# Kernel tuning notes

Hardware: AMD Instinct MI355X
Metric: run time of the kernel (lower is better)

The kernel has to match this reference:

```python
import jax, jax.numpy as jnp
import numpy as np

HEADS = 8
DIM = 512
DIM_HEAD = DIM // 8        # 64
M = DIM // 2               # 256 landmarks
PINV_ITERS = 6
KERNEL = 33                # residual depthwise conv kernel (33,1)


def moore_penrose_pinv(x, iters):
    # x: [b, h, m, m]; Newton-Schulz style iterative pseudoinverse (lucidrains impl)
    abs_x = jnp.abs(x)
    col = abs_x.sum(axis=-1)
    row = abs_x.sum(axis=-2)
    z = jnp.swapaxes(x, -1, -2) / (jnp.max(col) * jnp.max(row))
    I = jnp.eye(x.shape[-1], dtype=x.dtype)
    for _ in range(iters):
        xz = x @ z
        z = 0.25 * z @ (13.0 * I - xz @ (15.0 * I - xz @ (7.0 * I - xz)))
    return z


def setup_inputs() -> dict:
    key = jax.random.key(0)
    ks = jax.random.split(key, 5)
    b, n, dim = 4, 8192, DIM
    x = jax.random.normal(ks[0], (b, n, dim), dtype=jnp.float32)
    # to_qkv: Linear(dim, 3*inner_dim, bias=False); inner_dim = heads*dim_head = dim
    w_qkv = jax.random.normal(ks[1], (dim, 3 * dim), dtype=jnp.float32) / np.sqrt(dim)
    # to_out: Linear(inner_dim, dim) with bias (dropout = identity in eval)
    w_out = jax.random.normal(ks[2], (dim, dim), dtype=jnp.float32) / np.sqrt(dim)
    b_out = jax.random.normal(ks[3], (dim,), dtype=jnp.float32) * 0.01
    # res_conv: Conv2d(heads, heads, (33,1), padding=(16,0), groups=heads, bias=False)
    conv_w = jax.random.normal(ks[4], (HEADS, 1, KERNEL, 1), dtype=jnp.float32) / np.sqrt(KERNEL)
    return {"x": x, "w_qkv": w_qkv, "w_out": w_out, "b_out": b_out, "conv_w": conv_w}


def nystrom_attention(x, w_qkv, w_out, b_out, conv_w):
    b, n, dim = x.shape
    h, d, m = HEADS, DIM_HEAD, M
    # pad front so seq len divisible by num_landmarks (no-op for n=8192, m=256)
    pad = (m - n % m) % m
    xp = jnp.pad(x, ((0, 0), (pad, 0), (0, 0)))
    np_ = n + pad

    qkv = xp @ w_qkv                                   # [b, np, 3*dim]
    q, k, v = jnp.split(qkv, 3, axis=-1)
    to_heads = lambda t: t.reshape(b, np_, h, d).transpose(0, 2, 1, 3)  # [b,h,np,d]
    q, k, v = to_heads(q), to_heads(k), to_heads(v)
    q = q * (d ** -0.5)

    l = np_ // m                                       # tokens per landmark
    pool = lambda t: t.reshape(b, h, m, l, d).mean(axis=3)  # [b,h,m,d]
    q_l, k_l = pool(q), pool(k)

    attn1 = jax.nn.softmax(jnp.einsum('bhnd,bhmd->bhnm', q, k_l), axis=-1)    # [b,h,np,m]
    attn2 = jax.nn.softmax(jnp.einsum('bhid,bhjd->bhij', q_l, k_l), axis=-1)  # [b,h,m,m]
    attn3 = jax.nn.softmax(jnp.einsum('bhmd,bhnd->bhmn', q_l, k), axis=-1)    # [b,h,m,np]

    attn2_inv = moore_penrose_pinv(attn2, PINV_ITERS)
    out = (attn1 @ attn2_inv) @ (attn3 @ v)            # [b,h,np,d]

    # depthwise conv residual over the sequence axis, per head
    res = jax.lax.conv_general_dilated(
        v, conv_w, window_strides=(1, 1),
        padding=((KERNEL // 2, KERNEL // 2), (0, 0)),
        dimension_numbers=('NCHW', 'OIHW', 'NCHW'),
        feature_group_count=h)
    out = out + res

    out = out.transpose(0, 2, 1, 3).reshape(b, np_, dim)
    out = out @ w_out + b_out
    return out[:, -n:]


def reference(x, w_qkv, w_out, b_out, conv_w):
    return x + nystrom_attention(x, w_qkv, w_out, b_out, conv_w)
```

## Files before the change

kernel.cpp:

```cpp
#include <hip/hip_runtime.h>


#define N_SEQ 8192
#define DMODEL 512
#define NHEAD 8
#define DHEAD 64
#define NLAND 256
#define BH 32

typedef unsigned short u16;
typedef __attribute__((ext_vector_type(8))) short bh8;
typedef __attribute__((ext_vector_type(4))) float fx4;

__device__ __forceinline__ float bf2f(u16 u) { return __uint_as_float(((unsigned)u) << 16); }
__device__ __forceinline__ u16 f2bf(float f) {
    unsigned x = __float_as_uint(f);
    return (u16)((x + 0x7fffu + ((x >> 16) & 1u)) >> 16);
}
__device__ __forceinline__ fx4 mfma16(bh8 a, bh8 b, fx4 c) {
    return __builtin_amdgcn_mfma_f32_16x16x32_bf16(a, b, c, 0, 0, 0);
}

__global__ void detect_kernel(const u16* __restrict__ X, unsigned* flag_out)
{
    __shared__ int cnt;
    if (threadIdx.x == 0) cnt = 0;
    __syncthreads();
    u16 u = X[threadIdx.x * 2];
    int e = (u >> 7) & 0xFF;
    int insane = (u != 0) && (e < 90 || e > 140);
    atomicAdd(&cnt, insane);
    __syncthreads();
    if (threadIdx.x == 0) flag_out[0] = (cnt > 64) ? 1u : 0u;
}

__global__ __launch_bounds__(256) void convert_kernel(
    const void* __restrict__ in, u16* __restrict__ out, int n, const unsigned* __restrict__ flag)
{
    int i = blockIdx.x * 256 + threadIdx.x;
    if (i >= n) return;
    if (flag[0]) out[i] = f2bf(((const float*)in)[i]);
    else         out[i] = ((const u16*)in)[i];
}

__global__ __launch_bounds__(256) void wtrans_kernel(
    const void* __restrict__ in, u16* __restrict__ out, int rows, int cols,
    const unsigned* __restrict__ flag)
{
    int idx = blockIdx.x * 256 + threadIdx.x;
    if (idx >= rows * cols) return;
    int r = idx / cols, c = idx % cols;
    float v = flag[0] ? ((const float*)in)[idx] : bf2f(((const u16*)in)[idx]);
    out[(size_t)c * rows + r] = f2bf(v);
}

__global__ __launch_bounds__(256) void f2b_kernel(const float* __restrict__ in, u16* __restrict__ out, int n)
{
    int i = blockIdx.x * 256 + threadIdx.x;
    if (i < n) out[i] = f2bf(in[i]);
}

__global__ __launch_bounds__(256) void qkv_mfma_kernel(
    const u16* __restrict__ X, const u16* __restrict__ WT,
    u16* __restrict__ Q, u16* __restrict__ K, u16* __restrict__ VT)
{
    __shared__ u16 Xs[128 * 40];
    __shared__ u16 Ws[128 * 40];
    const int tid = threadIdx.x;
    const int wave = tid >> 6, lane = tid & 63;
    const int wrow = (wave >> 1) * 64, wcol = (wave & 1) * 64;
    const int i0 = blockIdx.x * 128;
    const int j0 = blockIdx.y * 128;
    const int lr = tid >> 2, lk = (tid & 3) * 8;
    const int lm = lane & 15, lq = lane >> 4;
    fx4 acc[4][4];
#pragma unroll
    for (int a = 0; a < 4; ++a)
#pragma unroll
        for (int b = 0; b < 4; ++b) acc[a][b] = (fx4){0.f, 0.f, 0.f, 0.f};

    for (int k0 = 0; k0 < DMODEL; k0 += 32) {
        uint4 x0 = *(const uint4*)(X + (size_t)(i0 + lr) * DMODEL + k0 + lk);
        uint4 x1 = *(const uint4*)(X + (size_t)(i0 + 64 + lr) * DMODEL + k0 + lk);
        uint4 w0 = *(const uint4*)(WT + (size_t)(j0 + lr) * DMODEL + k0 + lk);
        uint4 w1 = *(const uint4*)(WT + (size_t)(j0 + 64 + lr) * DMODEL + k0 + lk);
        __syncthreads();
        *(uint4*)(Xs + lr * 40 + lk) = x0;
        *(uint4*)(Xs + (64 + lr) * 40 + lk) = x1;
        *(uint4*)(Ws + lr * 40 + lk) = w0;
        *(uint4*)(Ws + (64 + lr) * 40 + lk) = w1;
        __syncthreads();
        bh8 xf[4], wf[4];
#pragma unroll
        for (int im = 0; im < 4; ++im)
            xf[im] = *(const bh8*)(Xs + (wrow + im * 16 + lm) * 40 + lq * 8);
#pragma unroll
        for (int in = 0; in < 4; ++in)
            wf[in] = *(const bh8*)(Ws + (wcol + in * 16 + lm) * 40 + lq * 8);
#pragma unroll
        for (int im = 0; im < 4; ++im)
#pragma unroll
            for (int in = 0; in < 4; ++in)
                acc[im][in] = mfma16(wf[in], xf[im], acc[im][in]);
    }
#pragma unroll
    for (int im = 0; im < 4; ++im) {
        int m = i0 + wrow + im * 16 + lm;
        int bb = m >> 13, ns = m & (N_SEQ - 1);
#pragma unroll
        for (int in = 0; in < 4; ++in) {
            int nn = j0 + wcol + in * 16 + (lq << 2);
            int which = nn >> 9;
            int h = (nn >> 6) & 7;
            int d = nn & 63;
            if (which == 2) {
                size_t vb = (size_t)(bb * NHEAD + h) * DHEAD;
#pragma unroll
                for (int cc = 0; cc < 4; ++cc)
                    VT[(vb + d + cc) * N_SEQ + ns] = f2bf(acc[im][in][cc]);
            } else {
                u16* dst = (which == 0) ? Q : K;
                float sc = (which == 0) ? 0.125f : 1.f;
                ushort4 o;
                o.x = f2bf(acc[im][in][0] * sc); o.y = f2bf(acc[im][in][1] * sc);
                o.z = f2bf(acc[im][in][2] * sc); o.w = f2bf(acc[im][in][3] * sc);
                *(ushort4*)(dst + ((size_t)(bb * NHEAD + h) * N_SEQ + ns) * DHEAD + d) = o;
            }
        }
    }
}

__global__ __launch_bounds__(64) void pool_kernel(
    const u16* __restrict__ Q, const u16* __restrict__ K,
    float* __restrict__ QL, float* __restrict__ KL,
    u16* __restrict__ QLb, u16* __restrict__ KLb)
{
    int m = blockIdx.x, bh = blockIdx.y, d = threadIdx.x;
    size_t base = ((size_t)bh * N_SEQ + m * 32) * DHEAD + d;
    float sq = 0.f, sk = 0.f;
#pragma unroll
    for (int i = 0; i < 32; ++i) {
        sq += bf2f(Q[base + i * DHEAD]);
        sk += bf2f(K[base + i * DHEAD]);
    }
    size_t ob = ((size_t)bh * NLAND + m) * DHEAD + d;
    sq *= (1.f / 32.f); sk *= (1.f / 32.f);
    QL[ob] = sq; KL[ob] = sk;
    QLb[ob] = f2bf(sq); KLb[ob] = f2bf(sk);
}

__global__ __launch_bounds__(256) void attn2_kernel(
    const float* __restrict__ QL, const float* __restrict__ KL, float* __restrict__ A2)
{
    __shared__ float qrow[64];
    __shared__ float red[256];
    int i = blockIdx.x, bh = blockIdx.y, j = threadIdx.x;
    if (j < 64) qrow[j] = QL[((size_t)bh * NLAND + i) * DHEAD + j];
    __syncthreads();
    const float* kr = KL + ((size_t)bh * NLAND + j) * DHEAD;
    float lg = 0.f;
#pragma unroll
    for (int d = 0; d < 64; ++d) lg += qrow[d] * kr[d];
    red[j] = lg; __syncthreads();
    for (int s = 128; s > 0; s >>= 1) { if (j < s) red[j] = fmaxf(red[j], red[j + s]); __syncthreads(); }
    float mx = red[0]; __syncthreads();
    float p = __expf(lg - mx);
    red[j] = p; __syncthreads();
    for (int s = 128; s > 0; s >>= 1) { if (j < s) red[j] += red[j + s]; __syncthreads(); }
    float sum = red[0];
    A2[((size_t)bh * NLAND + i) * NLAND + j] = p / sum;
}

__global__ void init_scal_kernel(unsigned* scal) { if (threadIdx.x < 2) scal[threadIdx.x] = 0u; }

__global__ __launch_bounds__(256) void absmax_kernel(const float* __restrict__ A2, unsigned* scal)
{
    __shared__ float red[256];
    int bh = blockIdx.x, t = threadIdx.x;
    const float* Ab = A2 + (size_t)bh * 65536;
    float cs = 0.f, rs = 0.f;
    for (int j = 0; j < 256; ++j) cs += fabsf(Ab[t * 256 + j]);
    for (int i = 0; i < 256; ++i) rs += fabsf(Ab[i * 256 + t]);
    red[t] = cs; __syncthreads();
    for (int s = 128; s > 0; s >>= 1) { if (t < s) red[t] = fmaxf(red[t], red[t + s]); __syncthreads(); }
    if (t == 0) atomicMax(scal + 0, __float_as_uint(red[0]));
    __syncthreads();
    red[t] = rs; __syncthreads();
    for (int s = 128; s > 0; s >>= 1) { if (t < s) red[t] = fmaxf(red[t], red[t + s]); __syncthreads(); }
    if (t == 0) atomicMax(scal + 1, __float_as_uint(red[0]));
}

__global__ __launch_bounds__(256) void z0_kernel(
    const float* __restrict__ A2, const unsigned* __restrict__ scal,
    u16* __restrict__ zb, u16* __restrict__ zbT)
{
    float inv = 1.f / (__uint_as_float(scal[0]) * __uint_as_float(scal[1]));
    size_t idx = (size_t)blockIdx.x * 256 + threadIdx.x;
    size_t bh = idx >> 16;
    int r = (int)(idx & 65535);
    int i = r >> 8, j = r & 255;
    zb[idx]  = f2bf(A2[(bh << 16) + (size_t)j * 256 + i] * inv);
    zbT[idx] = f2bf(A2[idx] * inv);
}

__global__ __launch_bounds__(256) void bgemm_mfma_kernel(
    const u16* __restrict__ A, const u16* __restrict__ BT,
    u16* __restrict__ Cn, u16* __restrict__ Ct, const u16* __restrict__ E,
    int N, long sB, long sCn, long sCt, float sc, float alpha, float beta, int wn, int wt)
{
    __shared__ u16 As[64 * 40];
    __shared__ u16 Bs[64 * 40];
    const int tid = threadIdx.x;
    const int wave = tid >> 6, lane = tid & 63;
    const int wm = (wave >> 1) * 32, wnn = (wave & 1) * 32;
    const int i0 = blockIdx.x * 64, j0 = blockIdx.y * 64, bh = blockIdx.z;
    const u16* Ab = A + (size_t)bh * 65536;
    const u16* Bb = BT + (size_t)bh * sB;
    const int lr = tid >> 2, lk = (tid & 3) * 8;
    const int lm = lane & 15, lq = lane >> 4;
    fx4 acc[2][2];
#pragma unroll
    for (int a = 0; a < 2; ++a)
#pragma unroll
        for (int b = 0; b < 2; ++b) acc[a][b] = (fx4){0.f, 0.f, 0.f, 0.f};

    for (int k0 = 0; k0 < 256; k0 += 32) {
        uint4 a4 = *(const uint4*)(Ab + (size_t)(i0 + lr) * 256 + k0 + lk);
        uint4 b4 = *(const uint4*)(Bb + (size_t)(j0 + lr) * 256 + k0 + lk);
        __syncthreads();
        *(uint4*)(As + lr * 40 + lk) = a4;
        *(uint4*)(Bs + lr * 40 + lk) = b4;
        __syncthreads();
        bh8 lf[2], rf[2];
#pragma unroll
        for (int im = 0; im < 2; ++im)
            lf[im] = *(const bh8*)(As + (wm + im * 16 + lm) * 40 + lq * 8);
#pragma unroll
        for (int in = 0; in < 2; ++in)
            rf[in] = *(const bh8*)(Bs + (wnn + in * 16 + lm) * 40 + lq * 8);
#pragma unroll
        for (int im = 0; im < 2; ++im)
#pragma unroll
            for (int in = 0; in < 2; ++in)
                acc[im][in] = mfma16(lf[im], rf[in], acc[im][in]);
    }
#pragma unroll
    for (int im = 0; im < 2; ++im) {
#pragma unroll
        for (int in = 0; in < 2; ++in) {
            int n = j0 + wnn + in * 16 + lm;
            int m0 = i0 + wm + im * 16 + (lq << 2);
            float c[4];
#pragma unroll
            for (int r = 0; r < 4; ++r) {
                int m = m0 + r;
                float x = beta * acc[im][in][r];
                if (alpha != 0.f)
                    x += alpha * bf2f(E[(size_t)bh * 65536 + (size_t)m * 256 + n]);
                if (m == n) x += sc;
                c[r] = x;
            }
            if (wn) {
#pragma unroll
                for (int r = 0; r < 4; ++r)
                    Cn[(size_t)bh * sCn + (size_t)(m0 + r) * N + n] = f2bf(c[r]);
            }
            if (wt) {
                ushort4 o;
                o.x = f2bf(c[0]); o.y = f2bf(c[1]); o.z = f2bf(c[2]); o.w = f2bf(c[3]);
                *(ushort4*)(Ct + (size_t)bh * sCt + (size_t)n * 256 + m0) = o;
            }
        }
    }
}

__global__ __launch_bounds__(256) void attn3v_mfma_kernel(
    const u16* __restrict__ QLb, const u16* __restrict__ Kb,
    const u16* __restrict__ VTb, u16* __restrict__ PO, float* __restrict__ ML)
{
    __shared__ u16 Pl[4][32 * 72];
    const int tid = threadIdx.x;
    const int wave = tid >> 6, lane = tid & 63;
    const int q = lane >> 4, l15 = lane & 15;
    const int m0 = blockIdx.x * 32;
    const int part = blockIdx.y * 4 + wave;
    const int bh = blockIdx.z;
    const int nbase = part * 512;
    u16* Pw = Pl[wave];
    bh8 qf[2][2];
#pragma unroll
    for (int mt = 0; mt < 2; ++mt)
#pragma unroll
        for (int ks = 0; ks < 2; ++ks)
            qf[mt][ks] = *(const bh8*)(QLb + ((size_t)bh * NLAND + m0 + mt * 16 + l15) * DHEAD + ks * 32 + q * 8);
    float M[2] = {-1e30f, -1e30f};
    float L[2] = {0.f, 0.f};
    fx4 O[2][4];
#pragma unroll
    for (int mt = 0; mt < 2; ++mt)
#pragma unroll
        for (int dt = 0; dt < 4; ++dt) O[mt][dt] = (fx4){0.f, 0.f, 0.f, 0.f};

    for (int c = 0; c < 8; ++c) {
        const int n0 = nbase + c * 64;
        fx4 S[4][2];
#pragma unroll
        for (int nt = 0; nt < 4; ++nt)
#pragma unroll
            for (int mt = 0; mt < 2; ++mt) S[nt][mt] = (fx4){0.f, 0.f, 0.f, 0.f};
#pragma unroll
        for (int ks = 0; ks < 2; ++ks)
#pragma unroll
            for (int nt = 0; nt < 4; ++nt) {
                bh8 kf = *(const bh8*)(Kb + ((size_t)bh * N_SEQ + n0 + nt * 16 + l15) * DHEAD + ks * 32 + q * 8);
                S[nt][0] = mfma16(kf, qf[0][ks], S[nt][0]);
                S[nt][1] = mfma16(kf, qf[1][ks], S[nt][1]);
            }
#pragma unroll
        for (int mt = 0; mt < 2; ++mt) {
            float cm = -1e30f;
#pragma unroll
            for (int nt = 0; nt < 4; ++nt)
#pragma unroll
                for (int r = 0; r < 4; ++r) cm = fmaxf(cm, S[nt][mt][r]);
            cm = fmaxf(cm, __shfl_xor(cm, 16));
            cm = fmaxf(cm, __shfl_xor(cm, 32));
            float Mn = fmaxf(M[mt], cm);
            float al = __expf(M[mt] - Mn);
            M[mt] = Mn;
            L[mt] *= al;
#pragma unroll
            for (int dt = 0; dt < 4; ++dt) {
                O[mt][dt][0] *= al; O[mt][dt][1] *= al;
                O[mt][dt][2] *= al; O[mt][dt][3] *= al;
            }
            float ps = 0.f;
#pragma unroll
            for (int nt = 0; nt < 4; ++nt)
#pragma unroll
                for (int r = 0; r < 4; ++r) {
                    float p = __expf(S[nt][mt][r] - Mn);
                    ps += p;
                    Pw[(mt * 16 + l15) * 72 + nt * 16 + q * 4 + r] = f2bf(p);
                }
            ps += __shfl_xor(ps, 16);
            ps += __shfl_xor(ps, 32);
            L[mt] += ps;
        }
#pragma unroll
        for (int ks = 0; ks < 2; ++ks) {
            bh8 pf[2];
#pragma unroll
            for (int mt = 0; mt < 2; ++mt)
                pf[mt] = *(const bh8*)(Pw + (mt * 16 + l15) * 72 + ks * 32 + q * 8);
#pragma unroll
            for (int dt = 0; dt < 4; ++dt) {
                bh8 vf = *(const bh8*)(VTb + ((size_t)bh * DHEAD + dt * 16 + l15) * N_SEQ + n0 + ks * 32 + q * 8);
                O[0][dt] = mfma16(vf, pf[0], O[0][dt]);
                O[1][dt] = mfma16(vf, pf[1], O[1][dt]);
            }
        }
    }
#pragma unroll
    for (int mt = 0; mt < 2; ++mt) {
        size_t mrow = (size_t)(bh * 16 + part) * NLAND + m0 + mt * 16 + l15;
#pragma unroll
        for (int dt = 0; dt < 4; ++dt) {
            ushort4 o;
            o.x = f2bf(O[mt][dt][0]); o.y = f2bf(O[mt][dt][1]);
            o.z = f2bf(O[mt][dt][2]); o.w = f2bf(O[mt][dt][3]);
            *(ushort4*)(PO + mrow * DHEAD + dt * 16 + q * 4) = o;
        }
        if (q == 0) { ML[mrow * 2] = M[mt]; ML[mrow * 2 + 1] = L[mt]; }
    }
}

__global__ __launch_bounds__(64) void combine_kernel(
    const u16* __restrict__ PO, const float* __restrict__ ML, u16* __restrict__ W3VT)
{
    int m = blockIdx.x, bh = blockIdx.y, d = threadIdx.x;
    float Mg = -1e30f;
#pragma unroll
    for (int p = 0; p < 16; ++p)
        Mg = fmaxf(Mg, ML[((size_t)(bh * 16 + p) * NLAND + m) * 2]);
    float denom = 0.f, o = 0.f;
#pragma unroll
    for (int p = 0; p < 16; ++p) {
        size_t ix = (size_t)(bh * 16 + p) * NLAND + m;
        float w = __expf(ML[ix * 2] - Mg);
        denom += ML[ix * 2 + 1] * w;
        o += bf2f(PO[ix * DHEAD + d]) * w;
    }
    W3VT[((size_t)bh * DHEAD + d) * NLAND + m] = f2bf(o / denom);
}

__global__ __launch_bounds__(256) void outheads_mfma_kernel(
    const u16* __restrict__ Qb, const u16* __restrict__ KLb,
    const u16* __restrict__ WMT, const u16* __restrict__ VTb,
    const u16* __restrict__ CW, u16* __restrict__ Y)
{
    __shared__ u16 Pl[32 * 264];
    __shared__ u16 vsh[64 * 72];
    __shared__ float wmax[4][32], wsum[4][32];
    __shared__ float cws[33];
    const int tid = threadIdx.x;
    const int wave = tid >> 6, lane = tid & 63;
    const int q = lane >> 4, l15 = lane & 15;
    const int bh = blockIdx.y;
    const int bb = bh >> 3, h = bh & 7;
    const int n0 = blockIdx.x * 32;
#pragma unroll
    for (int e = 0; e < 16; ++e) {
        int d = wave * 16 + e;
        int gn = n0 - 16 + lane;
        u16 v = (gn >= 0 && gn < N_SEQ) ? VTb[((size_t)bh * DHEAD + d) * N_SEQ + gn] : (u16)0;
        vsh[lane * 72 + d] = v;
    }
    if (tid < 33) cws[tid] = bf2f(CW[h * 33 + tid]);
    fx4 S[2][4];
#pragma unroll
    for (int nt = 0; nt < 2; ++nt)
#pragma unroll
        for (int mt = 0; mt < 4; ++mt) S[nt][mt] = (fx4){0.f, 0.f, 0.f, 0.f};
#pragma unroll
    for (int ks = 0; ks < 2; ++ks) {
        bh8 qfr[2];
#pragma unroll
        for (int nt = 0; nt < 2; ++nt)
            qfr[nt] = *(const bh8*)(Qb + ((size_t)bh * N_SEQ + n0 + nt * 16 + l15) * DHEAD + ks * 32 + q * 8);
#pragma unroll
        for (int mt = 0; mt < 4; ++mt) {
            bh8 kf = *(const bh8*)(KLb + ((size_t)bh * NLAND + wave * 64 + mt * 16 + l15) * DHEAD + ks * 32 + q * 8);
            S[0][mt] = mfma16(qfr[0], kf, S[0][mt]);
            S[1][mt] = mfma16(qfr[1], kf, S[1][mt]);
        }
    }
#pragma unroll
    for (int nt = 0; nt < 2; ++nt)
#pragma unroll
        for (int r = 0; r < 4; ++r) {
            float pm = -1e30f;
#pragma unroll
            for (int mt = 0; mt < 4; ++mt) pm = fmaxf(pm, S[nt][mt][r]);
            pm = fmaxf(pm, __shfl_xor(pm, 1));
            pm = fmaxf(pm, __shfl_xor(pm, 2));
            pm = fmaxf(pm, __shfl_xor(pm, 4));
            pm = fmaxf(pm, __shfl_xor(pm, 8));
            if (l15 == 0) wmax[wave][nt * 16 + q * 4 + r] = pm;
        }
    __syncthreads();
#pragma unroll
    for (int nt = 0; nt < 2; ++nt)
#pragma unroll
        for (int r = 0; r < 4; ++r) {
            int nl = nt * 16 + q * 4 + r;
            float Mfull = fmaxf(fmaxf(wmax[0][nl], wmax[1][nl]), fmaxf(wmax[2][nl], wmax[3][nl]));
            float ps = 0.f;
#pragma unroll
            for (int mt = 0; mt < 4; ++mt) {
                float p = __expf(S[nt][mt][r] - Mfull);
                ps += p;
                Pl[nl * 264 + wave * 64 + mt * 16 + l15] = f2bf(p);
            }
            ps += __shfl_xor(ps, 1);
            ps += __shfl_xor(ps, 2);
            ps += __shfl_xor(ps, 4);
            ps += __shfl_xor(ps, 8);
            if (l15 == 0) wsum[wave][nl] = ps;
        }
    __syncthreads();
    fx4 O[2];
    O[0] = (fx4){0.f, 0.f, 0.f, 0.f};
    O[1] = (fx4){0.f, 0.f, 0.f, 0.f};
#pragma unroll
    for (int ks = 0; ks < 8; ++ks) {
        bh8 af = *(const bh8*)(WMT + ((size_t)bh * DHEAD + wave * 16 + l15) * NLAND + ks * 32 + q * 8);
#pragma unroll
        for (int nt = 0; nt < 2; ++nt) {
            bh8 pf = *(const bh8*)(Pl + (nt * 16 + l15) * 264 + ks * 32 + q * 8);
            O[nt] = mfma16(af, pf, O[nt]);
        }
    }
#pragma unroll
    for (int nt = 0; nt < 2; ++nt) {
        int nl = nt * 16 + l15;
        float inv = 1.f / (wsum[0][nl] + wsum[1][nl] + wsum[2][nl] + wsum[3][nl]);
        fx4 v = O[nt];
        v[0] *= inv; v[1] *= inv; v[2] *= inv; v[3] *= inv;
#pragma unroll
        for (int t = 0; t < 33; ++t) {
            float w = cws[t];
            const u16* vp = vsh + (nl + t) * 72 + wave * 16 + q * 4;
            v[0] += w * bf2f(vp[0]); v[1] += w * bf2f(vp[1]);
            v[2] += w * bf2f(vp[2]); v[3] += w * bf2f(vp[3]);
        }
        ushort4 o;
        o.x = f2bf(v[0]); o.y = f2bf(v[1]); o.z = f2bf(v[2]); o.w = f2bf(v[3]);
        *(ushort4*)(Y + ((size_t)bb * N_SEQ + n0 + nl) * DMODEL + h * DHEAD + wave * 16 + q * 4) = o;
    }
}

__global__ __launch_bounds__(256) void final_mfma_kernel(
    const u16* __restrict__ Y, const u16* __restrict__ WT,
    const u16* __restrict__ Bias, const u16* __restrict__ X, void* __restrict__ Out,
    const unsigned* __restrict__ flag)
{
    __shared__ u16 Xs[128 * 40];
    __shared__ u16 Ws[128 * 40];
    const int tid = threadIdx.x;
    const int wave = tid >> 6, lane = tid & 63;
    const int wrow = (wave >> 1) * 64, wcol = (wave & 1) * 64;
    const int i0 = blockIdx.x * 128;
    const int j0 = blockIdx.y * 128;
    const int lr = tid >> 2, lk = (tid & 3) * 8;
    const int lm = lane & 15, lq = lane >> 4;
    const unsigned isf32 = flag[0];
    fx4 acc[4][4];
#pragma unroll
    for (int a = 0; a < 4; ++a)
#pragma unroll
        for (int b = 0; b < 4; ++b) acc[a][b] = (fx4){0.f, 0.f, 0.f, 0.f};

    for (int k0 = 0; k0 < DMODEL; k0 += 32) {
        uint4 x0 = *(const uint4*)(Y + (size_t)(i0 + lr) * DMODEL + k0 + lk);
        uint4 x1 = *(const uint4*)(Y + (size_t)(i0 + 64 + lr) * DMODEL + k0 + lk);
        uint4 w0 = *(const uint4*)(WT + (size_t)(j0 + lr) * DMODEL + k0 + lk);
        uint4 w1 = *(const uint4*)(WT + (size_t)(j0 + 64 + lr) * DMODEL + k0 + lk);
        __syncthreads();
        *(uint4*)(Xs + lr * 40 + lk) = x0;
        *(uint4*)(Xs + (64 + lr) * 40 + lk) = x1;
        *(uint4*)(Ws + lr * 40 + lk) = w0;
        *(uint4*)(Ws + (64 + lr) * 40 + lk) = w1;
        __syncthreads();
        bh8 xf[4], wf[4];
#pragma unroll
        for (int im = 0; im < 4; ++im)
            xf[im] = *(const bh8*)(Xs + (wrow + im * 16 + lm) * 40 + lq * 8);
#pragma unroll
        for (int in = 0; in < 4; ++in)
            wf[in] = *(const bh8*)(Ws + (wcol + in * 16 + lm) * 40 + lq * 8);
#pragma unroll
        for (int im = 0; im < 4; ++im)
#pragma unroll
            for (int in = 0; in < 4; ++in)
                acc[im][in] = mfma16(wf[in], xf[im], acc[im][in]);
    }
#pragma unroll
    for (int im = 0; im < 4; ++im) {
        int m = i0 + wrow + im * 16 + lm;
#pragma unroll
        for (int in = 0; in < 4; ++in) {
            int nn = j0 + wcol + in * 16 + (lq << 2);
            ushort4 b4 = *(const ushort4*)(Bias + nn);
            ushort4 x4 = *(const ushort4*)(X + (size_t)m * DMODEL + nn);
            float c0 = acc[im][in][0] + bf2f(b4.x) + bf2f(x4.x);
            float c1 = acc[im][in][1] + bf2f(b4.y) + bf2f(x4.y);
            float c2 = acc[im][in][2] + bf2f(b4.z) + bf2f(x4.z);
            float c3 = acc[im][in][3] + bf2f(b4.w) + bf2f(x4.w);
            if (isf32) {
                *(float4*)((float*)Out + (size_t)m * DMODEL + nn) = make_float4(c0, c1, c2, c3);
            } else {
                ushort4 o;
                o.x = f2bf(c0); o.y = f2bf(c1); o.z = f2bf(c2); o.w = f2bf(c3);
                *(ushort4*)((u16*)Out + (size_t)m * DMODEL + nn) = o;
            }
        }
    }
}

extern "C" void kernel_launch(void* const* d_in, const int* in_sizes, int n_in,
                              void* d_out, int out_size, void* d_ws, size_t ws_size,
                              hipStream_t stream)
{
    (void)in_sizes; (void)n_in; (void)out_size; (void)ws_size;
    char* ws = (char*)d_ws;
    u16*   Xc    = (u16*)(ws + 0);
    u16*   WqkvT = (u16*)(ws + 33554432);
    u16*   WoutT = (u16*)(ws + 35127296);
    u16*   Boutc = (u16*)(ws + 35651584);
    u16*   CWc   = (u16*)(ws + 35652608);
    u16*   Qb    = (u16*)(ws + 35653632);
    u16*   Kb    = (u16*)(ws + 69208064);
    u16*   VTb   = (u16*)(ws + 102762496);
    float* QL    = (float*)(ws + 136316928);
    float* KL    = (float*)(ws + 138414080);
    u16*   QLb   = (u16*)(ws + 140511232);
    u16*   KLb   = (u16*)(ws + 141559808);
    u16*   W3VT  = (u16*)(ws + 142608384);
    u16*   WMT   = (u16*)(ws + 143656960);
    u16*   A2b   = (u16*)(ws + 144705536);
    u16*   zA    = (u16*)(ws + 148899840);
    u16*   zAT   = (u16*)(ws + 153094144);
    float* A2    = (float*)(ws + 157288448);
    u16*   PO    = (u16*)(ws + 157288448);
    float* ML    = (float*)(ws + 174065664);
    u16*   zB    = (u16*)(ws + 165677056);
    u16*   zBT   = (u16*)(ws + 169871360);
    u16*   xz    = (u16*)(ws + 174065664);
    u16*   xzT   = (u16*)(ws + 178259968);
    u16*   t2T   = (u16*)(ws + 182454272);
    u16*   t3T   = (u16*)(ws + 186648576);
    u16*   Yb    = (u16*)(ws + 157288448);
    unsigned* SCAL = (unsigned*)(ws + 190842880);

    detect_kernel<<<1, 256, 0, stream>>>((const u16*)d_in[0], SCAL + 2);
    convert_kernel<<<65536, 256, 0, stream>>>(d_in[0], Xc, 16777216, SCAL + 2);
    wtrans_kernel<<<3072, 256, 0, stream>>>(d_in[1], WqkvT, 512, 1536, SCAL + 2);
    wtrans_kernel<<<1024, 256, 0, stream>>>(d_in[2], WoutT, 512, 512, SCAL + 2);
    convert_kernel<<<2, 256, 0, stream>>>(d_in[3], Boutc, 512, SCAL + 2);
    convert_kernel<<<2, 256, 0, stream>>>(d_in[4], CWc, 264, SCAL + 2);

    qkv_mfma_kernel<<<dim3(256, 12), 256, 0, stream>>>(Xc, WqkvT, Qb, Kb, VTb);
    pool_kernel<<<dim3(256, BH), 64, 0, stream>>>(Qb, Kb, QL, KL, QLb, KLb);
    attn2_kernel<<<dim3(256, BH), 256, 0, stream>>>(QL, KL, A2);
    init_scal_kernel<<<1, 64, 0, stream>>>(SCAL);
    absmax_kernel<<<32, 256, 0, stream>>>(A2, SCAL);
    z0_kernel<<<8192, 256, 0, stream>>>(A2, SCAL, zA, zAT);
    f2b_kernel<<<8192, 256, 0, stream>>>(A2, A2b, 2097152);

    attn3v_mfma_kernel<<<dim3(8, 4, BH), 256, 0, stream>>>(QLb, Kb, VTb, PO, ML);
    combine_kernel<<<dim3(256, BH), 64, 0, stream>>>(PO, ML, W3VT);

    u16 *z = zA, *zT = zAT, *zn = zB, *znT = zBT;
    for (int it = 0; it < 6; ++it) {
        bgemm_mfma_kernel<<<dim3(4, 4, 32), 256, 0, stream>>>(
            A2b, zT, xz, xzT, A2b, 256, 65536, 65536, 65536, 0.f, 0.f, 1.f, 1, 1);
        bgemm_mfma_kernel<<<dim3(4, 4, 32), 256, 0, stream>>>(
            xz, xzT, xz, t2T, xz, 256, 65536, 65536, 65536, 15.f, -7.f, 1.f, 0, 1);
        bgemm_mfma_kernel<<<dim3(4, 4, 32), 256, 0, stream>>>(
            xz, t2T, xz, t3T, xz, 256, 65536, 65536, 65536, 13.f, 0.f, -1.f, 0, 1);
        bgemm_mfma_kernel<<<dim3(4, 4, 32), 256, 0, stream>>>(
            z, t3T, zn, znT, xz, 256, 65536, 65536, 65536, 0.f, 0.f, 0.25f, 1, 1);
        u16* t;
        t = z; z = zn; zn = t;
        t = zT; zT = znT; znT = t;
    }
    bgemm_mfma_kernel<<<dim3(4, 1, 32), 256, 0, stream>>>(
        z, W3VT, WMT, WMT, xz, 64, 16384, 16384, 16384, 0.f, 0.f, 1.f, 0, 1);
    outheads_mfma_kernel<<<dim3(256, BH), 256, 0, stream>>>(Qb, KLb, WMT, VTb, CWc, Yb);
    final_mfma_kernel<<<dim3(256, 4), 256, 0, stream>>>(Yb, WoutT, Boutc, Xc, d_out, SCAL + 2);
}
```

Before: 847.5 us.

## Use direct global-to-LDS loads with swizzle in GEMMs and split out residual conv

The QKV and output GEMMs now use global_load_lds with an XOR-swizzled 64-wide K tile instead of register-staged loads into padded shared memory. The depthwise residual conv moves into a separate conv_kernel that writes RT into the now-unused K buffer. The output-heads kernel handles 64 tokens per block and just adds the precomputed RT. This cuts register staging and recomputation of the conv, at the cost of an extra kernel launch and an extra round-trip of the conv result through global memory.

```diff
diff --git a/kernel.cpp b/kernel.cpp
--- a/kernel.cpp
+++ b/kernel.cpp
@@ -19,6 +19,11 @@
 }
 __device__ __forceinline__ fx4 mfma16(bh8 a, bh8 b, fx4 c) {
     return __builtin_amdgcn_mfma_f32_16x16x32_bf16(a, b, c, 0, 0, 0);
+}
+__device__ __forceinline__ void gload16(u16* lds, const u16* g) {
+    __builtin_amdgcn_global_load_lds(
+        (const __attribute__((address_space(1))) unsigned int*)g,
+        (__attribute__((address_space(3))) unsigned int*)lds, 16, 0, 0);
 }
 
 __global__ void detect_kernel(const u16* __restrict__ X, unsigned* flag_out)
@@ -64,44 +69,48 @@
     const u16* __restrict__ X, const u16* __restrict__ WT,
     u16* __restrict__ Q, u16* __restrict__ K, u16* __restrict__ VT)
 {
-    __shared__ u16 Xs[128 * 40];
-    __shared__ u16 Ws[128 * 40];
+    __shared__ u16 Xs[128 * 64];
+    __shared__ u16 Ws[128 * 64];
     const int tid = threadIdx.x;
     const int wave = tid >> 6, lane = tid & 63;
     const int wrow = (wave >> 1) * 64, wcol = (wave & 1) * 64;
     const int i0 = blockIdx.x * 128;
     const int j0 = blockIdx.y * 128;
-    const int lr = tid >> 2, lk = (tid & 3) * 8;
+    const int la = lane >> 3, lb = lane & 7;
     const int lm = lane & 15, lq = lane >> 4;
+    const int sw = lm & 7;
+    const int sc = (lb ^ la) * 8;
     fx4 acc[4][4];
 #pragma unroll
     for (int a = 0; a < 4; ++a)
 #pragma unroll
         for (int b = 0; b < 4; ++b) acc[a][b] = (fx4){0.f, 0.f, 0.f, 0.f};
 
-    for (int k0 = 0; k0 < DMODEL; k0 += 32) {
-        uint4 x0 = *(const uint4*)(X + (size_t)(i0 + lr) * DMODEL + k0 + lk);
-        uint4 x1 = *(const uint4*)(X + (size_t)(i0 + 64 + lr) * DMODEL + k0 + lk);
-        uint4 w0 = *(const uint4*)(WT + (size_t)(j0 + lr) * DMODEL + k0 + lk);
-        uint4 w1 = *(const uint4*)(WT + (size_t)(j0 + 64 + lr) * DMODEL + k0 + lk);
+    for (int k0 = 0; k0 < DMODEL; k0 += 64) {
         __syncthreads();
-        *(uint4*)(Xs + lr * 40 + lk) = x0;
-        *(uint4*)(Xs + (64 + lr) * 40 + lk) = x1;
-        *(uint4*)(Ws + lr * 40 + lk) = w0;
-        *(uint4*)(Ws + (64 + lr) * 40 + lk) = w1;
+#pragma unroll
+        for (int jj = 0; jj < 4; ++jj) {
+            int rb = wave * 32 + jj * 8;
+            gload16(Xs + rb * 64, X + (size_t)(i0 + rb + la) * DMODEL + k0 + sc);
+            gload16(Ws + rb * 64, WT + (size_t)(j0 + rb + la) * DMODEL + k0 + sc);
+        }
         __syncthreads();
-        bh8 xf[4], wf[4];
-#pragma unroll
-        for (int im = 0; im < 4; ++im)
-            xf[im] = *(const bh8*)(Xs + (wrow + im * 16 + lm) * 40 + lq * 8);
-#pragma unroll
-        for (int in = 0; in < 4; ++in)
-            wf[in] = *(const bh8*)(Ws + (wcol + in * 16 + lm) * 40 + lq * 8);
-#pragma unroll
-        for (int im = 0; im < 4; ++im)
+#pragma unroll
+        for (int ks = 0; ks < 2; ++ks) {
+            const int po = ((ks * 4 + lq) ^ sw) * 8;
+            bh8 xf[4], wf[4];
+#pragma unroll
+            for (int im = 0; im < 4; ++im)
+                xf[im] = *(const bh8*)(Xs + (wrow + im * 16 + lm) * 64 + po);
 #pragma unroll
             for (int in = 0; in < 4; ++in)
-                acc[im][in] = mfma16(wf[in], xf[im], acc[im][in]);
+                wf[in] = *(const bh8*)(Ws + (wcol + in * 16 + lm) * 64 + po);
+#pragma unroll
+            for (int im = 0; im < 4; ++im)
+#pragma unroll
+                for (int in = 0; in < 4; ++in)
+                    acc[im][in] = mfma16(wf[in], xf[im], acc[im][in]);
+        }
     }
 #pragma unroll
     for (int im = 0; im < 4; ++im) {
@@ -120,10 +129,10 @@
                     VT[(vb + d + cc) * N_SEQ + ns] = f2bf(acc[im][in][cc]);
             } else {
                 u16* dst = (which == 0) ? Q : K;
-                float sc = (which == 0) ? 0.125f : 1.f;
+                float s = (which == 0) ? 0.125f : 1.f;
                 ushort4 o;
-                o.x = f2bf(acc[im][in][0] * sc); o.y = f2bf(acc[im][in][1] * sc);
-                o.z = f2bf(acc[im][in][2] * sc); o.w = f2bf(acc[im][in][3] * sc);
+                o.x = f2bf(acc[im][in][0] * s); o.y = f2bf(acc[im][in][1] * s);
+                o.z = f2bf(acc[im][in][2] * s); o.w = f2bf(acc[im][in][3] * s);
                 *(ushort4*)(dst + ((size_t)(bb * NHEAD + h) * N_SEQ + ns) * DHEAD + d) = o;
             }
         }
@@ -394,54 +403,80 @@
     W3VT[((size_t)bh * DHEAD + d) * NLAND + m] = f2bf(o / denom);
 }
 
+__global__ __launch_bounds__(256) void conv_kernel(
+    const u16* __restrict__ VT, const u16* __restrict__ CW, u16* __restrict__ RT)
+{
+    __shared__ float vl[2080];
+    __shared__ float cws[33];
+    const int tid = threadIdx.x;
+    const int c0 = blockIdx.x * 2048;
+    const int row = blockIdx.y;
+    const int h = (row >> 6) & 7;
+    const u16* src = VT + (size_t)row * N_SEQ;
+    for (int i = tid; i < 2080; i += 256) {
+        int gn = c0 - 16 + i;
+        vl[i] = (gn >= 0 && gn < N_SEQ) ? bf2f(src[gn]) : 0.f;
+    }
+    if (tid < 33) cws[tid] = bf2f(CW[h * 33 + tid]);
+    __syncthreads();
+    float v[40];
+    const int base = tid * 8;
+#pragma unroll
+    for (int i = 0; i < 40; ++i) v[i] = vl[base + i];
+    float s[8];
+#pragma unroll
+    for (int j = 0; j < 8; ++j) {
+        float a = 0.f;
+#pragma unroll
+        for (int t = 0; t < 33; ++t) a += cws[t] * v[j + t];
+        s[j] = a;
+    }
+    u16* dst = RT + (size_t)row * N_SEQ + c0 + base;
+    ushort4 o0, o1;
+    o0.x = f2bf(s[0]); o0.y = f2bf(s[1]); o0.z = f2bf(s[2]); o0.w = f2bf(s[3]);
+    o1.x = f2bf(s[4]); o1.y = f2bf(s[5]); o1.z = f2bf(s[6]); o1.w = f2bf(s[7]);
+    *(ushort4*)dst = o0;
+    *(ushort4*)(dst + 4) = o1;
+}
+
 __global__ __launch_bounds__(256) void outheads_mfma_kernel(
     const u16* __restrict__ Qb, const u16* __restrict__ KLb,
-    const u16* __restrict__ WMT, const u16* __restrict__ VTb,
-    const u16* __restrict__ CW, u16* __restrict__ Y)
-{
-    __shared__ u16 Pl[32 * 264];
-    __shared__ u16 vsh[64 * 72];
-    __shared__ float wmax[4][32], wsum[4][32];
-    __shared__ float cws[33];
+    const u16* __restrict__ WMT, const u16* __restrict__ RT,
+    u16* __restrict__ Y)
+{
+    __shared__ u16 Pl[64 * 264];
+    __shared__ float wmax[4][64];
+    __shared__ float wsum[4][64];
     const int tid = threadIdx.x;
     const int wave = tid >> 6, lane = tid & 63;
     const int q = lane >> 4, l15 = lane & 15;
     const int bh = blockIdx.y;
     const int bb = bh >> 3, h = bh & 7;
-    const int n0 = blockIdx.x * 32;
-#pragma unroll
-    for (int e = 0; e < 16; ++e) {
-        int d = wave * 16 + e;
-        int gn = n0 - 16 + lane;
-        u16 v = (gn >= 0 && gn < N_SEQ) ? VTb[((size_t)bh * DHEAD + d) * N_SEQ + gn] : (u16)0;
-        vsh[lane * 72 + d] = v;
-    }
-    if (tid < 33) cws[tid] = bf2f(CW[h * 33 + tid]);
-    fx4 S[2][4];
-#pragma unroll
-    for (int nt = 0; nt < 2; ++nt)
-#pragma unroll
-        for (int mt = 0; mt < 4; ++mt) S[nt][mt] = (fx4){0.f, 0.f, 0.f, 0.f};
+    const int n0 = blockIdx.x * 64;
+    fx4 S[4][4];
+#pragma unroll
+    for (int a = 0; a < 4; ++a)
+#pragma unroll
+        for (int b = 0; b < 4; ++b) S[a][b] = (fx4){0.f, 0.f, 0.f, 0.f};
 #pragma unroll
     for (int ks = 0; ks < 2; ++ks) {
-        bh8 qfr[2];
-#pragma unroll
-        for (int nt = 0; nt < 2; ++nt)
+        bh8 qfr[4];
+#pragma unroll
+        for (int nt = 0; nt < 4; ++nt)
             qfr[nt] = *(const bh8*)(Qb + ((size_t)bh * N_SEQ + n0 + nt * 16 + l15) * DHEAD + ks * 32 + q * 8);
 #pragma unroll
         for (int mt = 0; mt < 4; ++mt) {
             bh8 kf = *(const bh8*)(KLb + ((size_t)bh * NLAND + wave * 64 + mt * 16 + l15) * DHEAD + ks * 32 + q * 8);
-            S[0][mt] = mfma16(qfr[0], kf, S[0][mt]);
-            S[1][mt] = mfma16(qfr[1], kf, S[1][mt]);
-        }
-    }
-#pragma unroll
-    for (int nt = 0; nt < 2; ++nt)
+#pragma unroll
+            for (int nt = 0; nt < 4; ++nt)
+                S[nt][mt] = mfma16(qfr[nt], kf, S[nt][mt]);
+        }
+    }
+#pragma unroll
+    for (int nt = 0; nt < 4; ++nt)
 #pragma unroll
         for (int r = 0; r < 4; ++r) {
-            float pm = -1e30f;
-#pragma unroll
-            for (int mt = 0; mt < 4; ++mt) pm = fmaxf(pm, S[nt][mt][r]);
+            float pm = fmaxf(fmaxf(S[nt][0][r], S[nt][1][r]), fmaxf(S[nt][2][r], S[nt][3][r]));
             pm = fmaxf(pm, __shfl_xor(pm, 1));
             pm = fmaxf(pm, __shfl_xor(pm, 2));
             pm = fmaxf(pm, __shfl_xor(pm, 4));
@@ -450,15 +485,15 @@
         }
     __syncthreads();
 #pragma unroll
-    for (int nt = 0; nt < 2; ++nt)
+    for (int nt = 0; nt < 4; ++nt)
 #pragma unroll
         for (int r = 0; r < 4; ++r) {
             int nl = nt * 16 + q * 4 + r;
-            float Mfull = fmaxf(fmaxf(wmax[0][nl], wmax[1][nl]), fmaxf(wmax[2][nl], wmax[3][nl]));
+            float Mf = fmaxf(fmaxf(wmax[0][nl], wmax[1][nl]), fmaxf(wmax[2][nl], wmax[3][nl]));
             float ps = 0.f;
 #pragma unroll
             for (int mt = 0; mt < 4; ++mt) {
-                float p = __expf(S[nt][mt][r] - Mfull);
+                float p = __expf(S[nt][mt][r] - Mf);
                 ps += p;
                 Pl[nl * 264 + wave * 64 + mt * 16 + l15] = f2bf(p);
             }
@@ -469,34 +504,30 @@
             if (l15 == 0) wsum[wave][nl] = ps;
         }
     __syncthreads();
-    fx4 O[2];
-    O[0] = (fx4){0.f, 0.f, 0.f, 0.f};
-    O[1] = (fx4){0.f, 0.f, 0.f, 0.f};
+    fx4 O[4];
+#pragma unroll
+    for (int nt = 0; nt < 4; ++nt) O[nt] = (fx4){0.f, 0.f, 0.f, 0.f};
 #pragma unroll
     for (int ks = 0; ks < 8; ++ks) {
         bh8 af = *(const bh8*)(WMT + ((size_t)bh * DHEAD + wave * 16 + l15) * NLAND + ks * 32 + q * 8);
 #pragma unroll
-        for (int nt = 0; nt < 2; ++nt) {
-            bh8 pf = *(const bh8*)(Pl + (nt * 16 + l15) * 264 + ks * 32 + q * 8);
+        for (int nt = 0; nt < 4; ++nt) {
+            bh8 pf = *(const bh8*)(Pl + (size_t)(nt * 16 + l15) * 264 + ks * 32 + q * 8);
             O[nt] = mfma16(af, pf, O[nt]);
         }
     }
 #pragma unroll
-    for (int nt = 0; nt < 2; ++nt) {
+    for (int nt = 0; nt < 4; ++nt) {
         int nl = nt * 16 + l15;
         float inv = 1.f / (wsum[0][nl] + wsum[1][nl] + wsum[2][nl] + wsum[3][nl]);
+        int d0 = wave * 16 + (q << 2);
         fx4 v = O[nt];
-        v[0] *= inv; v[1] *= inv; v[2] *= inv; v[3] *= inv;
-#pragma unroll
-        for (int t = 0; t < 33; ++t) {
-            float w = cws[t];
-            const u16* vp = vsh + (nl + t) * 72 + wave * 16 + q * 4;
-            v[0] += w * bf2f(vp[0]); v[1] += w * bf2f(vp[1]);
-            v[2] += w * bf2f(vp[2]); v[3] += w * bf2f(vp[3]);
-        }
+#pragma unroll
+        for (int c = 0; c < 4; ++c)
+            v[c] = v[c] * inv + bf2f(RT[(size_t)(bh * DHEAD + d0 + c) * N_SEQ + n0 + nl]);
         ushort4 o;
         o.x = f2bf(v[0]); o.y = f2bf(v[1]); o.z = f2bf(v[2]); o.w = f2bf(v[3]);
-        *(ushort4*)(Y + ((size_t)bb * N_SEQ + n0 + nl) * DMODEL + h * DHEAD + wave * 16 + q * 4) = o;
+        *(ushort4*)(Y + ((size_t)bb * N_SEQ + n0 + nl) * DMODEL + h * DHEAD + d0) = o;
     }
 }
 
@@ -505,15 +536,17 @@
     const u16* __restrict__ Bias, const u16* __restrict__ X, void* __restrict__ Out,
     const unsigned* __restrict__ flag)
 {
-    __shared__ u16 Xs[128 * 40];
-    __shared__ u16 Ws[128 * 40];
+    __shared__ u16 Xs[128 * 64];
+    __shared__ u16 Ws[128 * 64];
     const int tid = threadIdx.x;
     const int wave = tid >> 6, lane = tid & 63;
     const int wrow = (wave >> 1) * 64, wcol = (wave & 1) * 64;
     const int i0 = blockIdx.x * 128;
     const int j0 = blockIdx.y * 128;
-    const int lr = tid >> 2, lk = (tid & 3) * 8;
+    const int la = lane >> 3, lb = lane & 7;
     const int lm = lane & 15, lq = lane >> 4;
+    const int sw = lm & 7;
+    const int sc = (lb ^ la) * 8;
     const unsigned isf32 = flag[0];
     fx4 acc[4][4];
 #pragma unroll
@@ -521,29 +554,31 @@
 #pragma unroll
         for (int b = 0; b < 4; ++b) acc[a][b] = (fx4){0.f, 0.f, 0.f, 0.f};
 
-    for (int k0 = 0; k0 < DMODEL; k0 += 32) {
-        uint4 x0 = *(const uint4*)(Y + (size_t)(i0 + lr) * DMODEL + k0 + lk);
-        uint4 x1 = *(const uint4*)(Y + (size_t)(i0 + 64 + lr) * DMODEL + k0 + lk);
-        uint4 w0 = *(const uint4*)(WT + (size_t)(j0 + lr) * DMODEL + k0 + lk);
-        uint4 w1 = *(const uint4*)(WT + (size_t)(j0 + 64 + lr) * DMODEL + k0 + lk);
+    for (int k0 = 0; k0 < DMODEL; k0 += 64) {
         __syncthreads();
-        *(uint4*)(Xs + lr * 40 + lk) = x0;
-        *(uint4*)(Xs + (64 + lr) * 40 + lk) = x1;
-        *(uint4*)(Ws + lr * 40 + lk) = w0;
-        *(uint4*)(Ws + (64 + lr) * 40 + lk) = w1;
+#pragma unroll
+        for (int jj = 0; jj < 4; ++jj) {
+            int rb = wave * 32 + jj * 8;
+            gload16(Xs + rb * 64, Y + (size_t)(i0 + rb + la) * DMODEL + k0 + sc);
+            gload16(Ws + rb * 64, WT + (size_t)(j0 + rb + la) * DMODEL + k0 + sc);
+        }
         __syncthreads();
-        bh8 xf[4], wf[4];
-#pragma unroll
-        for (int im = 0; im < 4; ++im)
-            xf[im] = *(const bh8*)(Xs + (wrow + im * 16 + lm) * 40 + lq * 8);
-#pragma unroll
-        for (int in = 0; in < 4; ++in)
-            wf[in] = *(const bh8*)(Ws + (wcol + in * 16 + lm) * 40 + lq * 8);
-#pragma unroll
-        for (int im = 0; im < 4; ++im)
+#pragma unroll
+        for (int ks = 0; ks < 2; ++ks) {
+            const int po = ((ks * 4 + lq) ^ sw) * 8;
+            bh8 xf[4], wf[4];
+#pragma unroll
+            for (int im = 0; im < 4; ++im)
+                xf[im] = *(const bh8*)(Xs + (wrow + im * 16 + lm) * 64 + po);
 #pragma unroll
             for (int in = 0; in < 4; ++in)
-                acc[im][in] = mfma16(wf[in], xf[im], acc[im][in]);
+                wf[in] = *(const bh8*)(Ws + (wcol + in * 16 + lm) * 64 + po);
+#pragma unroll
+            for (int im = 0; im < 4; ++im)
+#pragma unroll
+                for (int in = 0; in < 4; ++in)
+                    acc[im][in] = mfma16(wf[in], xf[im], acc[im][in]);
+        }
     }
 #pragma unroll
     for (int im = 0; im < 4; ++im) {
@@ -581,6 +616,7 @@
     u16*   CWc   = (u16*)(ws + 35652608);
     u16*   Qb    = (u16*)(ws + 35653632);
     u16*   Kb    = (u16*)(ws + 69208064);
+    u16*   RT    = (u16*)(ws + 69208064);
     u16*   VTb   = (u16*)(ws + 102762496);
     float* QL    = (float*)(ws + 136316928);
     float* KL    = (float*)(ws + 138414080);
@@ -620,6 +656,7 @@
 
     attn3v_mfma_kernel<<<dim3(8, 4, BH), 256, 0, stream>>>(QLb, Kb, VTb, PO, ML);
     combine_kernel<<<dim3(256, BH), 64, 0, stream>>>(PO, ML, W3VT);
+    conv_kernel<<<dim3(4, 2048), 256, 0, stream>>>(VTb, CWc, RT);
 
     u16 *z = zA, *zT = zAT, *zn = zB, *znT = zBT;
     for (int it = 0; it < 6; ++it) {
@@ -637,6 +674,6 @@
     }
     bgemm_mfma_kernel<<<dim3(4, 1, 32), 256, 0, stream>>>(
         z, W3VT, WMT, WMT, xz, 64, 16384, 16384, 16384, 0.f, 0.f, 1.f, 0, 1);
-    outheads_mfma_kernel<<<dim3(256, BH), 256, 0, stream>>>(Qb, KLb, WMT, VTb, CWc, Yb);
+    outheads_mfma_kernel<<<dim3(128, BH), 256, 0, stream>>>(Qb, KLb, WMT, RT, Yb);
     final_mfma_kernel<<<dim3(256, 4), 256, 0, stream>>>(Yb, WoutT, Boutc, Xc, d_out, SCAL + 2);
 }
```

Result: faster. 809.1 us (-4.5%).
